# Kernel tuning notes

Measured on AMD Instinct MI355X. Metric: run time of the kernel, lower is better.

Reference implementation:

```python
import jax, jax.numpy as jnp
import numpy as np

N_NODES = 50000
C = 256          # in_channels == hidden_size
E = 800000


def setup_inputs() -> dict:
    key = jax.random.key(0)
    ks = jax.random.split(key, 12)
    x = jax.random.normal(ks[0], (N_NODES, C), dtype=jnp.float32)
    edge_index = jax.random.randint(ks[1], (2, E), 0, N_NODES, dtype=jnp.int64)
    edge_attr = jax.random.uniform(ks[2], (E,), dtype=jnp.float32)
    edge_weights_index = jax.random.randint(ks[3], (2, E), 0, N_NODES, dtype=jnp.int64)
    s = 1.0 / np.sqrt(C)
    # TopKPooling projection vector
    p_pool = jax.random.normal(ks[4], (C,), dtype=jnp.float32) * s
    # GRU (input=C, hidden=C): gates stacked [r, z, n]
    W_ih = jax.random.normal(ks[5], (3 * C, C), dtype=jnp.float32) * s
    W_hh = jax.random.normal(ks[6], (3 * C, C), dtype=jnp.float32) * s
    b_ih = jnp.zeros((3 * C,), dtype=jnp.float32)
    b_hh = jnp.zeros((3 * C,), dtype=jnp.float32)
    # initial evolving GCN weight [C, C]
    W_init = jax.random.normal(ks[7], (C, C), dtype=jnp.float32) * s
    # EdgeDecoder MLP
    lin1_w = jax.random.normal(ks[8], (C, 2 * C), dtype=jnp.float32) / np.sqrt(2 * C)
    lin1_b = jnp.zeros((C,), dtype=jnp.float32)
    lin2_w = jax.random.normal(ks[9], (1, C), dtype=jnp.float32) * s
    lin2_b = jnp.zeros((1,), dtype=jnp.float32)
    return {
        "x": x, "edge_index": edge_index, "edge_attr": edge_attr,
        "edge_weights_index": edge_weights_index,
        "p_pool": p_pool, "W_ih": W_ih, "W_hh": W_hh, "b_ih": b_ih, "b_hh": b_hh,
        "W_init": W_init, "lin1_w": lin1_w, "lin1_b": lin1_b,
        "lin2_w": lin2_w, "lin2_b": lin2_b,
    }


def _forward(x, edge_attr, p_pool, W_ih, W_hh, b_ih, b_hh, W_init,
             lin1_w, lin1_b, lin2_w, lin2_b, edge_index, edge_weights_index):
    n_nodes, c = x.shape
    # --- EvolveGCNH: TopK pooling summary (k = in_channels) ---
    score = x @ p_pool / jnp.linalg.norm(p_pool)          # [N]
    top_score, perm = jax.lax.top_k(score, c)             # [C]
    x_tilde = x[perm] * jnp.tanh(top_score)[:, None]      # [C, C]
    # --- GRU step: input x_tilde (batch=C), hidden = evolving weight W_init ---
    gi = x_tilde @ W_ih.T + b_ih                           # [C, 3C]
    gh = W_init @ W_hh.T + b_hh                            # [C, 3C]
    i_r, i_z, i_n = jnp.split(gi, 3, axis=1)
    h_r, h_z, h_n = jnp.split(gh, 3, axis=1)
    r = jax.nn.sigmoid(i_r + h_r)
    z = jax.nn.sigmoid(i_z + h_z)
    n = jnp.tanh(i_n + r * h_n)
    W = (1.0 - z) * n + z * W_init                         # [C, C] evolved GCN weight
    # --- GCNConv with fixed W, add_self_loops=False ---
    xw = x @ W                                             # [N, C]
    src, dst = edge_index[0], edge_index[1]
    deg = jax.ops.segment_sum(edge_attr, dst, num_segments=n_nodes)
    dinv = jnp.where(deg > 0, jax.lax.rsqrt(jnp.where(deg > 0, deg, 1.0)), 0.0)
    norm = dinv[src] * edge_attr * dinv[dst]               # [E]
    node_emb = jax.ops.segment_sum(xw[src] * norm[:, None], dst,
                                   num_segments=n_nodes)   # [N, C]
    # --- EdgeDecoder: gather src/trg, concat, MLP ---
    s_idx, t_idx = edge_weights_index[0], edge_weights_index[1]
    edge_emb = jnp.concatenate([node_emb[s_idx], node_emb[t_idx]], axis=1)  # [E, 2C]
    h = jax.nn.relu(edge_emb @ lin1_w.T + lin1_b)          # [E, C]
    pred = h @ lin2_w.T + lin2_b                           # [E, 1]
    return pred.reshape(-1)


def reference(x, edge_index, edge_attr, edge_weights_index, p_pool,
              W_ih, W_hh, b_ih, b_hh, W_init, lin1_w, lin1_b, lin2_w, lin2_b):
    # dropout is identity in eval mode
    return _forward(x, edge_attr, p_pool, W_ih, W_hh, b_ih, b_hh, W_init,
                    lin1_w, lin1_b, lin2_w, lin2_b, edge_index, edge_weights_index)
```

## Files before the change

kernel.cpp:

```cpp
#include <hip/hip_runtime.h>
#include <hip/hip_bf16.h>
#include <math.h>


typedef __attribute__((ext_vector_type(8))) short bf16x8;
typedef __attribute__((ext_vector_type(8))) unsigned short u16x8;
typedef __attribute__((ext_vector_type(4))) float f32x4;

#define WSHIFT 9
#define WMASK 511
#define NBUCK 98

__device__ __forceinline__ unsigned f2key(float f) {
  unsigned u = __float_as_uint(f);
  return (u & 0x80000000u) ? ~u : (u | 0x80000000u);
}

__device__ __forceinline__ unsigned short f2bf(float f) {
  unsigned u = __float_as_uint(f);
  unsigned r = u + 0x7fffu + ((u >> 16) & 1u);
  return (unsigned short)(r >> 16);
}
__device__ __forceinline__ float bf2f(unsigned short h) {
  return __uint_as_float((unsigned)h << 16);
}

template <int CTRL>
__device__ __forceinline__ float dpp_add(float s) {
  int t = __builtin_amdgcn_update_dpp(0, __float_as_int(s), CTRL, 0xf, 0xf, false);
  return s + __int_as_float(t);
}

__device__ __forceinline__ void gload16(const void* g, void* l) {
  __builtin_amdgcn_global_load_lds((const __attribute__((address_space(1))) void*)g,
                                   (__attribute__((address_space(3))) void*)l, 16, 0, 0);
}

__global__ __launch_bounds__(256) void init_kernel(const float* __restrict__ lin1,
                                                   unsigned short* __restrict__ WAB,
                                                   int4* __restrict__ zb, int nz4) {
  int b = blockIdx.x, tid = threadIdx.x;
  if (b < 512) {
    int idx = b * 256 + tid;
    int n = idx >> 9, k = idx & 511;
    unsigned short h = f2bf(lin1[idx]);
    if (k < 256)
      WAB[n * 256 + k] = h;
    else
      WAB[(256 + n) * 256 + (k - 256)] = h;
  } else {
    int j = (b - 512) * 256 + tid;
    if (j < nz4) zb[j] = make_int4(0, 0, 0, 0);
  }
}

__global__ __launch_bounds__(256) void fusedA_kernel(const float* __restrict__ x,
                                                     const float* __restrict__ p,
                                                     float* __restrict__ score,
                                                     unsigned short* __restrict__ xh, int N,
                                                     const int* __restrict__ ei,
                                                     const int* __restrict__ ewi,
                                                     int* __restrict__ bcnt1,
                                                     int* __restrict__ bcnt2, int E) {
  int tid = threadIdx.x;
  if (blockIdx.x < 256) {
    __shared__ int c1[128], c2[128];
    if (tid < 128) { c1[tid] = 0; c2[tid] = 0; }
    __syncthreads();
    int idx = blockIdx.x * 256 + tid;
    int stride = 256 * 256;
    for (int e = idx; e < E; e += stride) {
      atomicAdd(&c1[ei[E + e] >> WSHIFT], 1);
      atomicAdd(&c2[ewi[e] >> WSHIFT], 1);
    }
    __syncthreads();
    if (tid < 128) {
      if (c1[tid]) atomicAdd(&bcnt1[tid], c1[tid]);
      if (c2[tid]) atomicAdd(&bcnt2[tid], c2[tid]);
    }
  } else {
    int node = (blockIdx.x - 256) * 4 + (tid >> 6);
    int lane = tid & 63;
    if (node >= N) return;
    float4 xv = ((const float4*)(x + (size_t)node * 256))[lane];
    ushort4 hv;
    hv.x = f2bf(xv.x);
    hv.y = f2bf(xv.y);
    hv.z = f2bf(xv.z);
    hv.w = f2bf(xv.w);
    ((ushort4*)(xh + (size_t)node * 256))[lane] = hv;
    float4 pv = ((const float4*)p)[lane];
    float s = xv.x * pv.x + xv.y * pv.y + xv.z * pv.z + xv.w * pv.w;
    float sp = pv.x * pv.x + pv.y * pv.y + pv.z * pv.z + pv.w * pv.w;
#pragma unroll
    for (int off = 32; off > 0; off >>= 1) {
      s += __shfl_down(s, off, 64);
      sp += __shfl_down(sp, off, 64);
    }
    if (lane == 0) score[node] = s / sqrtf(sp);
  }
}

__global__ __launch_bounds__(256) void fusedB_kernel(const float* __restrict__ score, int n,
                                                     int* __restrict__ gh,
                                                     const int* __restrict__ bcnt1,
                                                     const int* __restrict__ bcnt2,
                                                     int* __restrict__ bbase1,
                                                     int* __restrict__ bbase2,
                                                     int* __restrict__ gcur1,
                                                     int* __restrict__ gcur2,
                                                     int* __restrict__ rowp1,
                                                     int* __restrict__ rowp2, int N, int E) {
  int tid = threadIdx.x;
  if (blockIdx.x < 64) {
    __shared__ int lh[4096];
    for (int i = tid; i < 4096; i += 256) lh[i] = 0;
    __syncthreads();
    int idx = blockIdx.x * 256 + tid;
    int stride = 64 * 256;
    for (int i = idx; i < n; i += stride) {
      unsigned key = f2key(score[i]);
      atomicAdd(&lh[key >> 20], 1);
    }
    __syncthreads();
    for (int i = tid; i < 4096; i += 256) {
      int v = lh[i];
      if (v) atomicAdd(&gh[i], v);
    }
  } else {
    __shared__ int ss[128];
    int v = 0;
    if (tid < 128) { v = (tid < NBUCK) ? bcnt1[tid] : 0; ss[tid] = v; }
    __syncthreads();
    for (int off = 1; off < 128; off <<= 1) {
      int a = 0, b = 0;
      if (tid < 128) { a = ss[tid]; b = (tid >= off) ? ss[tid - off] : 0; }
      __syncthreads();
      if (tid < 128) ss[tid] = a + b;
      __syncthreads();
    }
    if (tid < 128) {
      int excl = ss[tid] - v;
      if (tid < NBUCK) { bbase1[tid] = excl; gcur1[tid] = excl; }
      if (tid == NBUCK - 1) bbase1[NBUCK] = excl + v;
    }
    __syncthreads();
    int v2 = 0;
    if (tid < 128) { v2 = (tid < NBUCK) ? bcnt2[tid] : 0; ss[tid] = v2; }
    __syncthreads();
    for (int off = 1; off < 128; off <<= 1) {
      int a = 0, b = 0;
      if (tid < 128) { a = ss[tid]; b = (tid >= off) ? ss[tid - off] : 0; }
      __syncthreads();
      if (tid < 128) ss[tid] = a + b;
      __syncthreads();
    }
    if (tid < 128) {
      int excl = ss[tid] - v2;
      if (tid < NBUCK) { bbase2[tid] = excl; gcur2[tid] = excl; }
      if (tid == NBUCK - 1) bbase2[NBUCK] = excl + v2;
    }
    if (tid == 0) { rowp1[N] = E; rowp2[N] = E; }
  }
}

__global__ __launch_bounds__(1024) void fusedC_kernel(const int* __restrict__ ei,
                                                      const float* __restrict__ attr,
                                                      int* __restrict__ gcur1,
                                                      int2* __restrict__ stage1,
                                                      const int* __restrict__ ewi,
                                                      int* __restrict__ gcur2,
                                                      int2* __restrict__ stage2,
                                                      int E, int nb,
                                                      const float* __restrict__ score, int n, int k,
                                                      const int* __restrict__ gh,
                                                      int* __restrict__ perm,
                                                      float* __restrict__ tts) {
  int tid = threadIdx.x;
  if ((int)blockIdx.x < 2 * nb) {
    bool conv = (int)blockIdx.x < nb;
    __shared__ int pcnt[128], pcur[128];
    int base = (conv ? blockIdx.x : blockIdx.x - nb) * 8192;
    int* gcur = conv ? gcur1 : gcur2;
    int2* stage = conv ? stage1 : stage2;
    if (tid < 128) pcnt[tid] = 0;
    __syncthreads();
    int bk[8];
    int2 pl[8];
#pragma unroll
    for (int i = 0; i < 8; ++i) {
      int e = base + i * 1024 + tid;
      bk[i] = -1;
      if (e < E) {
        if (conv) {
          int d = ei[E + e];
          int s = ei[e];
          bk[i] = d >> WSHIFT;
          pl[i] = make_int2(s | ((d & WMASK) << 16), __float_as_int(attr[e]));
        } else {
          int s = ewi[e];
          int d = ewi[E + e];
          bk[i] = s >> WSHIFT;
          pl[i] = make_int2(d | ((s & WMASK) << 16), e);
        }
        atomicAdd(&pcnt[bk[i]], 1);
      }
    }
    __syncthreads();
    if (tid < NBUCK) {
      int c = pcnt[tid];
      pcur[tid] = c ? atomicAdd(&gcur[tid], c) : 0;
    }
    __syncthreads();
#pragma unroll
    for (int i = 0; i < 8; ++i) {
      if (bk[i] >= 0) {
        int pos = atomicAdd(&pcur[bk[i]], 1);
        stage[pos] = pl[i];
      }
    }
  } else {
    __shared__ int part[1024];
    __shared__ unsigned sT;
    {
      int b0 = tid * 4;
      int s0 = gh[b0], s1 = gh[b0 + 1], s2 = gh[b0 + 2], s3 = gh[b0 + 3];
      part[tid] = s0 + s1 + s2 + s3;
      __syncthreads();
      for (int off = 1; off < 1024; off <<= 1) {
        int v = part[tid];
        int add = (tid + off < 1024) ? part[tid + off] : 0;
        __syncthreads();
        part[tid] = v + add;
        __syncthreads();
      }
      int sufChunk = part[tid];
      int sufNext = (tid < 1023) ? part[tid + 1] : 0;
      if (sufNext < k && sufChunk >= k) {
        int run = sufNext;
        int b;
        run += s3;
        if (run >= k) b = b0 + 3;
        else {
          run += s2;
          if (run >= k) b = b0 + 2;
          else {
            run += s1;
            b = (run >= k) ? b0 + 1 : b0;
          }
        }
        sT = ((unsigned)b) << 20;
      }
    }
    __syncthreads();
    unsigned T = sT;
    __shared__ unsigned keys[1024];
    __shared__ int idxs[1024];
    __shared__ int cnt;
    if (tid == 0) cnt = 0;
    keys[tid] = 0u;
    idxs[tid] = 0x7fffffff;
    __syncthreads();
    for (int i = tid; i < n; i += 1024) {
      unsigned key = f2key(score[i]);
      if (key >= T) {
        int p = atomicAdd(&cnt, 1);
        if (p < 1024) { keys[p] = key; idxs[p] = i; }
      }
    }
    __syncthreads();
    for (int size = 2; size <= 1024; size <<= 1) {
      for (int stride = size >> 1; stride > 0; stride >>= 1) {
        int j = tid ^ stride;
        if (j > tid) {
          unsigned ka = keys[tid], kb = keys[j];
          int ia = idxs[tid], ib = idxs[j];
          bool aBefore = (ka > kb) || (ka == kb && ia < ib);
          bool up = ((tid & size) == 0);
          if (aBefore != up) {
            keys[tid] = kb; keys[j] = ka;
            idxs[tid] = ib; idxs[j] = ia;
          }
        }
        __syncthreads();
      }
    }
    if (tid < k) {
      int idx = idxs[tid];
      perm[tid] = idx;
      tts[tid] = tanhf(score[idx]);
    }
  }
}

__global__ __launch_bounds__(256) void fusedD_kernel(const float* __restrict__ x,
                                                     const int* __restrict__ perm,
                                                     const float* __restrict__ tts,
                                                     const float* __restrict__ Wi,
                                                     const float* __restrict__ W_ih,
                                                     const float* __restrict__ W_hh,
                                                     const float* __restrict__ b_ih,
                                                     const float* __restrict__ b_hh,
                                                     unsigned short* __restrict__ WevoT,
                                                     const int2* __restrict__ stage1,
                                                     const int* __restrict__ bbase1,
                                                     int2* __restrict__ esv,
                                                     int* __restrict__ rowp1,
                                                     float* __restrict__ dinv,
                                                     const int2* __restrict__ stage2,
                                                     const int* __restrict__ bbase2,
                                                     int2* __restrict__ eto,
                                                     int* __restrict__ rowp2, int N) {
  int tid = threadIdx.x;
  if (blockIdx.x < 256) {
    int i = blockIdx.x, j = tid;
    __shared__ float sx[256], sh[256];
    sx[j] = x[(size_t)perm[i] * 256 + j] * tts[i];
    sh[j] = Wi[i * 256 + j];
    __syncthreads();
    float gi[3], gh[3];
#pragma unroll
    for (int g = 0; g < 3; ++g) {
      int row = g * 256 + j;
      const float4* wi4 = (const float4*)(W_ih + (size_t)row * 256);
      const float4* wh4 = (const float4*)(W_hh + (size_t)row * 256);
      float si = 0.f, s2 = 0.f;
      for (int k4 = 0; k4 < 64; ++k4) {
        float4 wv = wi4[k4];
        float4 hv = wh4[k4];
        int k = k4 * 4;
        si += sx[k] * wv.x + sx[k + 1] * wv.y + sx[k + 2] * wv.z + sx[k + 3] * wv.w;
        s2 += sh[k] * hv.x + sh[k + 1] * hv.y + sh[k + 2] * hv.z + sh[k + 3] * hv.w;
      }
      gi[g] = si + b_ih[row];
      gh[g] = s2 + b_hh[row];
    }
    float r = 1.f / (1.f + expf(-(gi[0] + gh[0])));
    float z = 1.f / (1.f + expf(-(gi[1] + gh[1])));
    float nn = tanhf(gi[2] + r * gh[2]);
    float w = (1.f - z) * nn + z * sh[j];
    WevoT[(size_t)j * 256 + i] = f2bf(w);
  } else {
    __shared__ int cnt[512];
    __shared__ float degs[512];
    __shared__ int pref[512];
    __shared__ int ss[256];
    int bb2 = blockIdx.x - 256;
    bool isConv = bb2 < NBUCK;
    int b = isConv ? bb2 : bb2 - NBUCK;
    const int2* stage = isConv ? stage1 : stage2;
    const int* bbase = isConv ? bbase1 : bbase2;
    int beg = bbase[b], end = bbase[b + 1];
    int node0 = b << WSHIFT;
    cnt[tid] = 0; cnt[tid + 256] = 0;
    degs[tid] = 0.f; degs[tid + 256] = 0.f;
    __syncthreads();
    for (int j = beg + tid; j < end; j += 256) {
      int2 p = stage[j];
      int loc = p.x >> 16;
      atomicAdd(&cnt[loc], 1);
      if (isConv) atomicAdd(&degs[loc], __int_as_float(p.y));
    }
    __syncthreads();
    int c0 = cnt[2 * tid], c1 = cnt[2 * tid + 1];
    ss[tid] = c0 + c1;
    __syncthreads();
    for (int off = 1; off < 256; off <<= 1) {
      int a = ss[tid];
      int bsum = (tid >= off) ? ss[tid - off] : 0;
      __syncthreads();
      ss[tid] = a + bsum;
      __syncthreads();
    }
    int excl = (tid ? ss[tid - 1] : 0);
    pref[2 * tid] = excl;
    pref[2 * tid + 1] = excl + c0;
    __syncthreads();
#pragma unroll
    for (int h = 0; h < 2; ++h) {
      int i = tid + h * 256;
      int node = node0 + i;
      if (node < N) {
        if (isConv) {
          rowp1[node] = beg + pref[i];
          float d = degs[i];
          dinv[node] = d > 0.f ? 1.f / sqrtf(d) : 0.f;
        } else {
          rowp2[node] = beg + pref[i];
        }
      }
    }
    __syncthreads();
    int2* outb = isConv ? esv : eto;
    for (int j = beg + tid; j < end; j += 256) {
      int2 p = stage[j];
      int loc = p.x >> 16;
      int pos = beg + atomicAdd(&pref[loc], 1);
      outb[pos] = make_int2(p.x & 0xFFFF, p.y);
    }
  }
}

__global__ __launch_bounds__(512) void mfma_gemm128(const unsigned short* __restrict__ A,
                                                    const unsigned short* __restrict__ BT,
                                                    unsigned short* __restrict__ C1,
                                                    unsigned short* __restrict__ C2,
                                                    int M) {
  __shared__ unsigned short sA[128 * 32];
  __shared__ unsigned short sB[256 * 32];
  int tid = threadIdx.x;
  int wave = tid >> 6, lane = tid & 63;
  int quad = lane >> 4, r16 = lane & 15;
  int wm = wave >> 2, wn = wave & 3;
  int mbase = blockIdx.x * 128;
  const unsigned short* Bt = BT + ((size_t)blockIdx.y << 16);
  unsigned short* Cout = blockIdx.y ? C2 : C1;

  int srow = tid >> 2, scolq = tid & 3;
  const unsigned short* gA = A + (size_t)(mbase + srow) * 256 + scolq * 8;
  const unsigned short* gB0 = Bt + (size_t)srow * 256 + scolq * 8;
  const unsigned short* gB1 = Bt + (size_t)(128 + srow) * 256 + scolq * 8;
  unsigned short* lA = sA + wave * 512;
  unsigned short* lB0 = sB + wave * 512;
  unsigned short* lB1 = sB + 4096 + wave * 512;

  f32x4 acc[4][4];
#pragma unroll
  for (int i = 0; i < 4; ++i)
#pragma unroll
    for (int j = 0; j < 4; ++j) acc[i][j] = (f32x4){0.f, 0.f, 0.f, 0.f};

  const unsigned short* pA = sA + (wm * 64 + r16) * 32 + quad * 8;
  const unsigned short* pB = sB + (wn * 64 + r16) * 32 + quad * 8;

  for (int k0 = 0; k0 < 256; k0 += 32) {
    if (k0) __syncthreads();
    gload16(gA + k0, lA);
    gload16(gB0 + k0, lB0);
    gload16(gB1 + k0, lB1);
    __syncthreads();
    bf16x8 af[4], bfr[4];
#pragma unroll
    for (int mt = 0; mt < 4; ++mt) af[mt] = *(const bf16x8*)(pA + mt * 512);
#pragma unroll
    for (int nt = 0; nt < 4; ++nt) bfr[nt] = *(const bf16x8*)(pB + nt * 512);
#pragma unroll
    for (int mt = 0; mt < 4; ++mt)
#pragma unroll
      for (int nt = 0; nt < 4; ++nt)
        acc[mt][nt] = __builtin_amdgcn_mfma_f32_16x16x32_bf16(af[mt], bfr[nt], acc[mt][nt], 0, 0, 0);
  }
#pragma unroll
  for (int mt = 0; mt < 4; ++mt) {
#pragma unroll
    for (int rr = 0; rr < 4; ++rr) {
      int grow = mbase + wm * 64 + mt * 16 + quad * 4 + rr;
      if (grow < M) {
#pragma unroll
        for (int nt = 0; nt < 4; ++nt)
          Cout[(size_t)grow * 256 + wn * 64 + nt * 16 + r16] = f2bf(acc[mt][nt][rr]);
      }
    }
  }
}

__global__ __launch_bounds__(256) void gcn_gather(const unsigned short* __restrict__ xw,
                                                  const int* __restrict__ row_ptr,
                                                  const int2* __restrict__ esv,
                                                  const float* __restrict__ dinv,
                                                  unsigned short* __restrict__ ne, int N) {
  int node = blockIdx.x * 4 + (threadIdx.x >> 6);
  int lane = threadIdx.x & 63;
  int g = lane & 15, q = lane >> 4;
  if (node >= N) return;
  int beg = row_ptr[node], end = row_ptr[node + 1];
  float acc[16];
#pragma unroll
  for (int c = 0; c < 16; ++c) acc[c] = 0.f;
  const unsigned short* xb = xw + g * 16;

  for (int cb = beg; cb < end; cb += 64) {
    int cend = cb + 64 < end ? cb + 64 : end;
    int me = cb + lane;
    int2 mm = (me < cend) ? esv[me] : make_int2(0, 0);
    int mx = mm.x;
    float mv = __int_as_float(mm.y) * dinv[mx];

    float vA = 0.f, vB = 0.f, vC = 0.f;
    u16x8 rAa, rAb, rBa, rBb, rCa, rCb;
    {
      int e = cb + q;
      int sx = __shfl(mx, q, 64);
      float tv = __shfl(mv, q, 64);
      vA = (e < cend) ? tv : 0.f;
      rAa = *(const u16x8*)(xb + (size_t)sx * 256);
      rAb = *(const u16x8*)(xb + (size_t)sx * 256 + 8);
    }
    if (cb + 4 < cend) {
      int e = cb + 4 + q;
      int sx = __shfl(mx, 4 + q, 64);
      float tv = __shfl(mv, 4 + q, 64);
      vB = (e < cend) ? tv : 0.f;
      rBa = *(const u16x8*)(xb + (size_t)sx * 256);
      rBb = *(const u16x8*)(xb + (size_t)sx * 256 + 8);
    } else { rBa = rAa; rBb = rAb; }
    if (cb + 8 < cend) {
      int e = cb + 8 + q;
      int sx = __shfl(mx, 8 + q, 64);
      float tv = __shfl(mv, 8 + q, 64);
      vC = (e < cend) ? tv : 0.f;
      rCa = *(const u16x8*)(xb + (size_t)sx * 256);
      rCb = *(const u16x8*)(xb + (size_t)sx * 256 + 8);
    } else { rCa = rAa; rCb = rAb; }

    for (int jb = cb; jb < cend; jb += 12) {
#pragma unroll
      for (int c = 0; c < 8; ++c) acc[c] += bf2f(rAa[c]) * vA;
#pragma unroll
      for (int c = 0; c < 8; ++c) acc[8 + c] += bf2f(rAb[c]) * vA;
      vA = 0.f;
      if (jb + 12 < cend) {
        int e = jb + 12 + q;
        int idx = (e - cb) & 63;
        int sx = __shfl(mx, idx, 64);
        float tv = __shfl(mv, idx, 64);
        vA = (e < cend) ? tv : 0.f;
        rAa = *(const u16x8*)(xb + (size_t)sx * 256);
        rAb = *(const u16x8*)(xb + (size_t)sx * 256 + 8);
      }
#pragma unroll
      for (int c = 0; c < 8; ++c) acc[c] += bf2f(rBa[c]) * vB;
#pragma unroll
      for (int c = 0; c < 8; ++c) acc[8 + c] += bf2f(rBb[c]) * vB;
      vB = 0.f;
      if (jb + 16 < cend) {
        int e = jb + 16 + q;
        int idx = (e - cb) & 63;
        int sx = __shfl(mx, idx, 64);
        float tv = __shfl(mv, idx, 64);
        vB = (e < cend) ? tv : 0.f;
        rBa = *(const u16x8*)(xb + (size_t)sx * 256);
        rBb = *(const u16x8*)(xb + (size_t)sx * 256 + 8);
      }
#pragma unroll
      for (int c = 0; c < 8; ++c) acc[c] += bf2f(rCa[c]) * vC;
#pragma unroll
      for (int c = 0; c < 8; ++c) acc[8 + c] += bf2f(rCb[c]) * vC;
      vC = 0.f;
      if (jb + 20 < cend) {
        int e = jb + 20 + q;
        int idx = (e - cb) & 63;
        int sx = __shfl(mx, idx, 64);
        float tv = __shfl(mv, idx, 64);
        vC = (e < cend) ? tv : 0.f;
        rCa = *(const u16x8*)(xb + (size_t)sx * 256);
        rCb = *(const u16x8*)(xb + (size_t)sx * 256 + 8);
      }
    }
  }
#pragma unroll
  for (int c = 0; c < 16; ++c) {
    acc[c] += __shfl_xor(acc[c], 16, 64);
    acc[c] += __shfl_xor(acc[c], 32, 64);
  }
  if (q == 0) {
    float dd = dinv[node];
    u16x8 o0, o1;
#pragma unroll
    for (int c = 0; c < 8; ++c) {
      o0[c] = f2bf(acc[c] * dd);
      o1[c] = f2bf(acc[8 + c] * dd);
    }
    *(u16x8*)(ne + (size_t)node * 256 + g * 16) = o0;
    *(u16x8*)(ne + (size_t)node * 256 + g * 16 + 8) = o1;
  }
}

__global__ __launch_bounds__(256) void edge_decode_csr(const unsigned short* __restrict__ A,
                                                       const unsigned short* __restrict__ Bm,
                                                       const int* __restrict__ row_ptr,
                                                       const int2* __restrict__ eto,
                                                       const float* __restrict__ b1,
                                                       const float* __restrict__ w2,
                                                       const float* __restrict__ b2,
                                                       float* __restrict__ out, int N) {
  int node = blockIdx.x * 4 + (threadIdx.x >> 6);
  int lane = threadIdx.x & 63;
  int g = lane & 15, q = lane >> 4;
  if (node >= N) return;
  int beg = row_ptr[node], end = row_ptr[node + 1];
  if (beg >= end) return;
  float a[16], w[16];
  {
    u16x8 a0 = *(const u16x8*)(A + (size_t)node * 256 + g * 16);
    u16x8 a1 = *(const u16x8*)(A + (size_t)node * 256 + g * 16 + 8);
    const float4* bp = (const float4*)(b1 + g * 16);
    const float4* wp = (const float4*)(w2 + g * 16);
#pragma unroll
    for (int i = 0; i < 4; ++i) {
      float4 bv = bp[i];
      float4 wv = wp[i];
      a[i * 4 + 0] = (i < 2 ? bf2f(a0[i * 4 + 0]) : bf2f(a1[i * 4 - 8])) + bv.x;
      a[i * 4 + 1] = (i < 2 ? bf2f(a0[i * 4 + 1]) : bf2f(a1[i * 4 - 7])) + bv.y;
      a[i * 4 + 2] = (i < 2 ? bf2f(a0[i * 4 + 2]) : bf2f(a1[i * 4 - 6])) + bv.z;
      a[i * 4 + 3] = (i < 2 ? bf2f(a0[i * 4 + 3]) : bf2f(a1[i * 4 - 5])) + bv.w;
      w[i * 4 + 0] = wv.x;
      w[i * 4 + 1] = wv.y;
      w[i * 4 + 2] = wv.z;
      w[i * 4 + 3] = wv.w;
    }
  }
  float base = b2[0];
  const unsigned short* Bb = Bm + g * 16;

  for (int cb = beg; cb < end; cb += 64) {
    int cend = cb + 64 < end ? cb + 64 : end;
    int me = cb + lane;
    int2 mm = (me < cend) ? eto[me] : make_int2(0, 0);
    int mx = mm.x, my = mm.y;

    bool okA = false, okB = false, okC = false;
    int oA = 0, oB = 0, oC = 0;
    u16x8 rAa, rAb, rBa, rBb, rCa, rCb;
    {
      int e = cb + q;
      int sx = __shfl(mx, q, 64);
      oA = __shfl(my, q, 64);
      okA = e < cend;
      rAa = *(const u16x8*)(Bb + (size_t)sx * 256);
      rAb = *(const u16x8*)(Bb + (size_t)sx * 256 + 8);
    }
    if (cb + 4 < cend) {
      int e = cb + 4 + q;
      int sx = __shfl(mx, 4 + q, 64);
      oB = __shfl(my, 4 + q, 64);
      okB = e < cend;
      rBa = *(const u16x8*)(Bb + (size_t)sx * 256);
      rBb = *(const u16x8*)(Bb + (size_t)sx * 256 + 8);
    } else { rBa = rAa; rBb = rAb; }
    if (cb + 8 < cend) {
      int e = cb + 8 + q;
      int sx = __shfl(mx, 8 + q, 64);
      oC = __shfl(my, 8 + q, 64);
      okC = e < cend;
      rCa = *(const u16x8*)(Bb + (size_t)sx * 256);
      rCb = *(const u16x8*)(Bb + (size_t)sx * 256 + 8);
    } else { rCa = rAa; rCb = rAb; }

    for (int jb = cb; jb < cend; jb += 12) {
      {
        float s0 = 0.f, s1 = 0.f;
#pragma unroll
        for (int c = 0; c < 8; ++c) s0 += fmaxf(a[c] + bf2f(rAa[c]), 0.f) * w[c];
#pragma unroll
        for (int c = 0; c < 8; ++c) s1 += fmaxf(a[8 + c] + bf2f(rAb[c]), 0.f) * w[8 + c];
        float s = s0 + s1;
        s = dpp_add<0x128>(s);
        s = dpp_add<0x124>(s);
        s = dpp_add<0x122>(s);
        s = dpp_add<0x121>(s);
        if (g == 0 && okA) out[oA] = s + base;
      }
      okA = false;
      if (jb + 12 < cend) {
        int e = jb + 12 + q;
        int idx = (e - cb) & 63;
        int sx = __shfl(mx, idx, 64);
        oA = __shfl(my, idx, 64);
        okA = e < cend;
        rAa = *(const u16x8*)(Bb + (size_t)sx * 256);
        rAb = *(const u16x8*)(Bb + (size_t)sx * 256 + 8);
      }
      {
        float s0 = 0.f, s1 = 0.f;
#pragma unroll
        for (int c = 0; c < 8; ++c) s0 += fmaxf(a[c] + bf2f(rBa[c]), 0.f) * w[c];
#pragma unroll
        for (int c = 0; c < 8; ++c) s1 += fmaxf(a[8 + c] + bf2f(rBb[c]), 0.f) * w[8 + c];
        float s = s0 + s1;
        s = dpp_add<0x128>(s);
        s = dpp_add<0x124>(s);
        s = dpp_add<0x122>(s);
        s = dpp_add<0x121>(s);
        if (g == 0 && okB) out[oB] = s + base;
      }
      okB = false;
      if (jb + 16 < cend) {
        int e = jb + 16 + q;
        int idx = (e - cb) & 63;
        int sx = __shfl(mx, idx, 64);
        oB = __shfl(my, idx, 64);
        okB = e < cend;
        rBa = *(const u16x8*)(Bb + (size_t)sx * 256);
        rBb = *(const u16x8*)(Bb + (size_t)sx * 256 + 8);
      }
      {
        float s0 = 0.f, s1 = 0.f;
#pragma unroll
        for (int c = 0; c < 8; ++c) s0 += fmaxf(a[c] + bf2f(rCa[c]), 0.f) * w[c];
#pragma unroll
        for (int c = 0; c < 8; ++c) s1 += fmaxf(a[8 + c] + bf2f(rCb[c]), 0.f) * w[8 + c];
        float s = s0 + s1;
        s = dpp_add<0x128>(s);
        s = dpp_add<0x124>(s);
        s = dpp_add<0x122>(s);
        s = dpp_add<0x121>(s);
        if (g == 0 && okC) out[oC] = s + base;
      }
      okC = false;
      if (jb + 20 < cend) {
        int e = jb + 20 + q;
        int idx = (e - cb) & 63;
        int sx = __shfl(mx, idx, 64);
        oC = __shfl(my, idx, 64);
        okC = e < cend;
        rCa = *(const u16x8*)(Bb + (size_t)sx * 256);
        rCb = *(const u16x8*)(Bb + (size_t)sx * 256 + 8);
      }
    }
  }
}

extern "C" void kernel_launch(void* const* d_in, const int* in_sizes, int n_in,
                              void* d_out, int out_size, void* d_ws, size_t ws_size,
                              hipStream_t stream) {
  const float* x      = (const float*)d_in[0];
  const int*   ei     = (const int*)d_in[1];
  const float* attr   = (const float*)d_in[2];
  const int*   ewi    = (const int*)d_in[3];
  const float* p_pool = (const float*)d_in[4];
  const float* W_ih   = (const float*)d_in[5];
  const float* W_hh   = (const float*)d_in[6];
  const float* b_ih   = (const float*)d_in[7];
  const float* b_hh   = (const float*)d_in[8];
  const float* W_init = (const float*)d_in[9];
  const float* lin1_w = (const float*)d_in[10];
  const float* lin1_b = (const float*)d_in[11];
  const float* lin2_w = (const float*)d_in[12];
  const float* lin2_b = (const float*)d_in[13];
  float* out = (float*)d_out;

  const int C = 256;
  const int N = in_sizes[0] / C;
  const int E = in_sizes[2];

  char* ws = (char*)d_ws;
  size_t off = 0;
  auto alloc = [&](size_t bytes) {
    size_t o = off;
    off = (off + bytes + 255) & ~(size_t)255;
    return o;
  };
  float*          score  = (float*)(ws + alloc((size_t)N * 4));
  int*            perm   = (int*)(ws + alloc(C * 4));
  float*          tts    = (float*)(ws + alloc(C * 4));
  unsigned short* WevoT  = (unsigned short*)(ws + alloc((size_t)C * C * 2));
  unsigned short* WAB    = (unsigned short*)(ws + alloc((size_t)2 * C * C * 2));
  int   zeroInts = 4096 + 128 + 128;
  char* zbase    = ws + alloc((size_t)zeroInts * 4);
  int* ghist = (int*)zbase;
  int* bcnt1 = (int*)(zbase + 4096 * 4);
  int* bcnt2 = (int*)(zbase + 4096 * 4 + 128 * 4);
  int*            bbase1 = (int*)(ws + alloc((NBUCK + 1) * 4));
  int*            bbase2 = (int*)(ws + alloc((NBUCK + 1) * 4));
  int*            gcur1  = (int*)(ws + alloc(128 * 4));
  int*            gcur2  = (int*)(ws + alloc(128 * 4));
  float*          dinv   = (float*)(ws + alloc((size_t)N * 4));
  int*            rowp1  = (int*)(ws + alloc((size_t)(N + 1) * 4));
  int*            rowp2  = (int*)(ws + alloc((size_t)(N + 1) * 4));
  int2*           stage1 = (int2*)(ws + alloc((size_t)E * 8));
  int2*           stage2 = (int2*)(ws + alloc((size_t)E * 8));
  int2*           esv    = (int2*)(ws + alloc((size_t)E * 8));
  int2*           eto    = (int2*)(ws + alloc((size_t)E * 8));
  unsigned short* xh     = (unsigned short*)(ws + alloc((size_t)N * C * 2));
  unsigned short* xwh    = (unsigned short*)(ws + alloc((size_t)N * C * 2));
  unsigned short* Bbf    = (unsigned short*)(ws + alloc((size_t)N * C * 2));
  unsigned short* ne  = xh;
  unsigned short* Abf = xwh;

  int nz4 = (zeroInts + 3) / 4;
  int nbP1 = (E + 8191) / 8192;

  init_kernel<<<512 + (nz4 + 255) / 256, 256, 0, stream>>>(lin1_w, WAB, (int4*)zbase, nz4);

  fusedA_kernel<<<256 + (N + 3) / 4, 256, 0, stream>>>(x, p_pool, score, xh, N,
                                                       ei, ewi, bcnt1, bcnt2, E);

  fusedB_kernel<<<65, 256, 0, stream>>>(score, N, ghist, bcnt1, bcnt2,
                                        bbase1, bbase2, gcur1, gcur2,
                                        rowp1, rowp2, N, E);

  fusedC_kernel<<<2 * nbP1 + 1, 1024, 0, stream>>>(ei, attr, gcur1, stage1,
                                                   ewi, gcur2, stage2, E, nbP1,
                                                   score, N, C, ghist, perm, tts);

  fusedD_kernel<<<256 + 2 * NBUCK, 256, 0, stream>>>(x, perm, tts, W_init,
                                                     W_ih, W_hh, b_ih, b_hh, WevoT,
                                                     stage1, bbase1, esv, rowp1, dinv,
                                                     stage2, bbase2, eto, rowp2, N);

  mfma_gemm128<<<dim3((N + 127) / 128, 1), 512, 0, stream>>>(xh, WevoT, xwh, xwh, N);

  gcn_gather<<<(N + 3) / 4, 256, 0, stream>>>(xwh, rowp1, esv, dinv, ne, N);

  mfma_gemm128<<<dim3((N + 127) / 128, 2), 512, 0, stream>>>(ne, WAB, Abf, Bbf, N);

  edge_decode_csr<<<(N + 3) / 4, 256, 0, stream>>>(Abf, Bbf, rowp2, eto,
                                                   lin1_b, lin2_w, lin2_b, out, N);
}
```

Measured before the change: 405.6 us.

## Reassociate GCN and decoder GEMMs, fold evolved weight into lin1, drop atomics

The GCN aggregation now runs on raw bf16 x instead of x@W, and the evolved weight W is folded into the decoder's lin1 halves via a small 256x256 product (PAB = lin1_half·W). This removes one full N×C GEMM pass and its intermediate buffer. The init kernel is merged into fusedA, and the global atomic histograms are replaced by per-block partial histograms that are summed later. This removes the zeroing step and the atomic contention, at the cost of extra reads in fusedB and fusedC and different bf16 rounding order.

Measured after the change: 447.8 us. 1.1x slower.

```diff
diff --git a/kernel.cpp b/kernel.cpp
--- a/kernel.cpp
+++ b/kernel.cpp
@@ -36,50 +36,20 @@
                                    (__attribute__((address_space(3))) void*)l, 16, 0, 0);
 }
 
-__global__ __launch_bounds__(256) void init_kernel(const float* __restrict__ lin1,
-                                                   unsigned short* __restrict__ WAB,
-                                                   int4* __restrict__ zb, int nz4) {
-  int b = blockIdx.x, tid = threadIdx.x;
-  if (b < 512) {
-    int idx = b * 256 + tid;
-    int n = idx >> 9, k = idx & 511;
-    unsigned short h = f2bf(lin1[idx]);
-    if (k < 256)
-      WAB[n * 256 + k] = h;
-    else
-      WAB[(256 + n) * 256 + (k - 256)] = h;
-  } else {
-    int j = (b - 512) * 256 + tid;
-    if (j < nz4) zb[j] = make_int4(0, 0, 0, 0);
-  }
-}
-
 __global__ __launch_bounds__(256) void fusedA_kernel(const float* __restrict__ x,
                                                      const float* __restrict__ p,
                                                      float* __restrict__ score,
-                                                     unsigned short* __restrict__ xh, int N,
+                                                     unsigned short* __restrict__ xh, int N, int NS,
                                                      const int* __restrict__ ei,
                                                      const int* __restrict__ ewi,
-                                                     int* __restrict__ bcnt1,
-                                                     int* __restrict__ bcnt2, int E) {
+                                                     int* __restrict__ bh1p,
+                                                     int* __restrict__ bh2p, int E,
+                                                     const float* __restrict__ lin1,
+                                                     unsigned short* __restrict__ WAB) {
   int tid = threadIdx.x;
-  if (blockIdx.x < 256) {
-    __shared__ int c1[128], c2[128];
-    if (tid < 128) { c1[tid] = 0; c2[tid] = 0; }
-    __syncthreads();
-    int idx = blockIdx.x * 256 + tid;
-    int stride = 256 * 256;
-    for (int e = idx; e < E; e += stride) {
-      atomicAdd(&c1[ei[E + e] >> WSHIFT], 1);
-      atomicAdd(&c2[ewi[e] >> WSHIFT], 1);
-    }
-    __syncthreads();
-    if (tid < 128) {
-      if (c1[tid]) atomicAdd(&bcnt1[tid], c1[tid]);
-      if (c2[tid]) atomicAdd(&bcnt2[tid], c2[tid]);
-    }
-  } else {
-    int node = (blockIdx.x - 256) * 4 + (tid >> 6);
+  int b = blockIdx.x;
+  if (b < NS) {
+    int node = b * 4 + (tid >> 6);
     int lane = tid & 63;
     if (node >= N) return;
     float4 xv = ((const float4*)(x + (size_t)node * 256))[lane];
@@ -98,13 +68,37 @@
       sp += __shfl_down(sp, off, 64);
     }
     if (lane == 0) score[node] = s / sqrtf(sp);
+  } else if (b < NS + 256) {
+    __shared__ int c1[128], c2[128];
+    int bb = b - NS;
+    if (tid < 128) { c1[tid] = 0; c2[tid] = 0; }
+    __syncthreads();
+    int idx = bb * 256 + tid;
+    int stride = 256 * 256;
+    for (int e = idx; e < E; e += stride) {
+      atomicAdd(&c1[ei[E + e] >> WSHIFT], 1);
+      atomicAdd(&c2[ewi[e] >> WSHIFT], 1);
+    }
+    __syncthreads();
+    if (tid < 128) {
+      bh1p[bb * 128 + tid] = c1[tid];
+      bh2p[bb * 128 + tid] = c2[tid];
+    }
+  } else {
+    int idx = (b - NS - 256) * 256 + tid;
+    int n = idx >> 9, k = idx & 511;
+    unsigned short h = f2bf(lin1[idx]);
+    if (k < 256)
+      WAB[n * 256 + k] = h;
+    else
+      WAB[(256 + n) * 256 + (k - 256)] = h;
   }
 }
 
 __global__ __launch_bounds__(256) void fusedB_kernel(const float* __restrict__ score, int n,
-                                                     int* __restrict__ gh,
-                                                     const int* __restrict__ bcnt1,
-                                                     const int* __restrict__ bcnt2,
+                                                     int* __restrict__ ghp,
+                                                     const int* __restrict__ bh1p,
+                                                     const int* __restrict__ bh2p,
                                                      int* __restrict__ bbase1,
                                                      int* __restrict__ bbase2,
                                                      int* __restrict__ gcur1,
@@ -123,20 +117,22 @@
       atomicAdd(&lh[key >> 20], 1);
     }
     __syncthreads();
-    for (int i = tid; i < 4096; i += 256) {
-      int v = lh[i];
-      if (v) atomicAdd(&gh[i], v);
-    }
+    int* row = ghp + blockIdx.x * 4096;
+    for (int i = tid; i < 4096; i += 256) row[i] = lh[i];
   } else {
     __shared__ int ss[128];
     int v = 0;
-    if (tid < 128) { v = (tid < NBUCK) ? bcnt1[tid] : 0; ss[tid] = v; }
+    if (tid < 128) {
+      if (tid < NBUCK)
+        for (int r = 0; r < 256; ++r) v += bh1p[r * 128 + tid];
+      ss[tid] = v;
+    }
     __syncthreads();
     for (int off = 1; off < 128; off <<= 1) {
-      int a = 0, b = 0;
-      if (tid < 128) { a = ss[tid]; b = (tid >= off) ? ss[tid - off] : 0; }
+      int a = 0, bsum = 0;
+      if (tid < 128) { a = ss[tid]; bsum = (tid >= off) ? ss[tid - off] : 0; }
       __syncthreads();
-      if (tid < 128) ss[tid] = a + b;
+      if (tid < 128) ss[tid] = a + bsum;
       __syncthreads();
     }
     if (tid < 128) {
@@ -146,13 +142,17 @@
     }
     __syncthreads();
     int v2 = 0;
-    if (tid < 128) { v2 = (tid < NBUCK) ? bcnt2[tid] : 0; ss[tid] = v2; }
+    if (tid < 128) {
+      if (tid < NBUCK)
+        for (int r = 0; r < 256; ++r) v2 += bh2p[r * 128 + tid];
+      ss[tid] = v2;
+    }
     __syncthreads();
     for (int off = 1; off < 128; off <<= 1) {
-      int a = 0, b = 0;
-      if (tid < 128) { a = ss[tid]; b = (tid >= off) ? ss[tid - off] : 0; }
+      int a = 0, bsum = 0;
+      if (tid < 128) { a = ss[tid]; bsum = (tid >= off) ? ss[tid - off] : 0; }
       __syncthreads();
-      if (tid < 128) ss[tid] = a + b;
+      if (tid < 128) ss[tid] = a + bsum;
       __syncthreads();
     }
     if (tid < 128) {
@@ -173,7 +173,7 @@
                                                       int2* __restrict__ stage2,
                                                       int E, int nb,
                                                       const float* __restrict__ score, int n, int k,
-                                                      const int* __restrict__ gh,
+                                                      const int* __restrict__ ghp,
                                                       int* __restrict__ perm,
                                                       float* __restrict__ tts) {
   int tid = threadIdx.x;
@@ -222,9 +222,14 @@
   } else {
     __shared__ int part[1024];
     __shared__ unsigned sT;
+    int s0, s1, s2, s3;
     {
       int b0 = tid * 4;
-      int s0 = gh[b0], s1 = gh[b0 + 1], s2 = gh[b0 + 2], s3 = gh[b0 + 3];
+      s0 = 0; s1 = 0; s2 = 0; s3 = 0;
+      for (int r = 0; r < 64; ++r) {
+        int4 v4 = *(const int4*)(ghp + r * 4096 + b0);
+        s0 += v4.x; s1 += v4.y; s2 += v4.z; s3 += v4.w;
+      }
       part[tid] = s0 + s1 + s2 + s3;
       __syncthreads();
       for (int off = 1; off < 1024; off <<= 1) {
@@ -240,13 +245,13 @@
         int run = sufNext;
         int b;
         run += s3;
-        if (run >= k) b = b0 + 3;
+        if (run >= k) b = tid * 4 + 3;
         else {
           run += s2;
-          if (run >= k) b = b0 + 2;
+          if (run >= k) b = tid * 4 + 2;
           else {
             run += s1;
-            b = (run >= k) ? b0 + 1 : b0;
+            b = (run >= k) ? tid * 4 + 1 : tid * 4;
           }
         }
         sT = ((unsigned)b) << 20;
@@ -301,7 +306,7 @@
                                                      const float* __restrict__ W_hh,
                                                      const float* __restrict__ b_ih,
                                                      const float* __restrict__ b_hh,
-                                                     unsigned short* __restrict__ WevoT,
+                                                     unsigned short* __restrict__ Wr,
                                                      const int2* __restrict__ stage1,
                                                      const int* __restrict__ bbase1,
                                                      int2* __restrict__ esv,
@@ -339,7 +344,7 @@
     float z = 1.f / (1.f + expf(-(gi[1] + gh[1])));
     float nn = tanhf(gi[2] + r * gh[2]);
     float w = (1.f - z) * nn + z * sh[j];
-    WevoT[(size_t)j * 256 + i] = f2bf(w);
+    Wr[(size_t)i * 256 + j] = f2bf(w);
   } else {
     __shared__ int cnt[512];
     __shared__ float degs[512];
@@ -401,83 +406,63 @@
   }
 }
 
-__global__ __launch_bounds__(512) void mfma_gemm128(const unsigned short* __restrict__ A,
-                                                    const unsigned short* __restrict__ BT,
-                                                    unsigned short* __restrict__ C1,
-                                                    unsigned short* __restrict__ C2,
-                                                    int M) {
-  __shared__ unsigned short sA[128 * 32];
-  __shared__ unsigned short sB[256 * 32];
+__global__ __launch_bounds__(256) void fusedE_kernel(const unsigned short* __restrict__ xh,
+                                                     const int* __restrict__ row_ptr,
+                                                     const int2* __restrict__ esv,
+                                                     const float* __restrict__ dinv,
+                                                     unsigned short* __restrict__ agg, int N, int NSB,
+                                                     const unsigned short* __restrict__ WAB,
+                                                     const unsigned short* __restrict__ Wr,
+                                                     unsigned short* __restrict__ PAB) {
   int tid = threadIdx.x;
-  int wave = tid >> 6, lane = tid & 63;
-  int quad = lane >> 4, r16 = lane & 15;
-  int wm = wave >> 2, wn = wave & 3;
-  int mbase = blockIdx.x * 128;
-  const unsigned short* Bt = BT + ((size_t)blockIdx.y << 16);
-  unsigned short* Cout = blockIdx.y ? C2 : C1;
-
-  int srow = tid >> 2, scolq = tid & 3;
-  const unsigned short* gA = A + (size_t)(mbase + srow) * 256 + scolq * 8;
-  const unsigned short* gB0 = Bt + (size_t)srow * 256 + scolq * 8;
-  const unsigned short* gB1 = Bt + (size_t)(128 + srow) * 256 + scolq * 8;
-  unsigned short* lA = sA + wave * 512;
-  unsigned short* lB0 = sB + wave * 512;
-  unsigned short* lB1 = sB + 4096 + wave * 512;
-
-  f32x4 acc[4][4];
-#pragma unroll
-  for (int i = 0; i < 4; ++i)
-#pragma unroll
-    for (int j = 0; j < 4; ++j) acc[i][j] = (f32x4){0.f, 0.f, 0.f, 0.f};
-
-  const unsigned short* pA = sA + (wm * 64 + r16) * 32 + quad * 8;
-  const unsigned short* pB = sB + (wn * 64 + r16) * 32 + quad * 8;
-
-  for (int k0 = 0; k0 < 256; k0 += 32) {
-    if (k0) __syncthreads();
-    gload16(gA + k0, lA);
-    gload16(gB0 + k0, lB0);
-    gload16(gB1 + k0, lB1);
-    __syncthreads();
-    bf16x8 af[4], bfr[4];
-#pragma unroll
-    for (int mt = 0; mt < 4; ++mt) af[mt] = *(const bf16x8*)(pA + mt * 512);
-#pragma unroll
-    for (int nt = 0; nt < 4; ++nt) bfr[nt] = *(const bf16x8*)(pB + nt * 512);
+  int lane = tid & 63;
+  if ((int)blockIdx.x >= NSB) {
+    int cb = blockIdx.x - NSB;
+    int by = cb >> 2, mb = cb & 3;
+    int wave = tid >> 6;
+    int quad = lane >> 4, r16 = lane & 15;
+    int n0 = wave * 64;
+    int mbase = mb * 64;
+    const unsigned short* A = WAB + ((size_t)by << 16);
+    f32x4 acc[4][4];
+#pragma unroll
+    for (int i = 0; i < 4; ++i)
+#pragma unroll
+      for (int j = 0; j < 4; ++j) acc[i][j] = (f32x4){0.f, 0.f, 0.f, 0.f};
+    for (int k0 = 0; k0 < 256; k0 += 32) {
+      int koff = k0 + quad * 8;
+      bf16x8 af[4], bfr[4];
+#pragma unroll
+      for (int mt = 0; mt < 4; ++mt)
+        af[mt] = *(const bf16x8*)(A + (size_t)(mbase + mt * 16 + r16) * 256 + koff);
+#pragma unroll
+      for (int nt = 0; nt < 4; ++nt)
+        bfr[nt] = *(const bf16x8*)(Wr + (size_t)(n0 + nt * 16 + r16) * 256 + koff);
+#pragma unroll
+      for (int mt = 0; mt < 4; ++mt)
+#pragma unroll
+        for (int nt = 0; nt < 4; ++nt)
+          acc[mt][nt] = __builtin_amdgcn_mfma_f32_16x16x32_bf16(af[mt], bfr[nt], acc[mt][nt], 0, 0, 0);
+    }
 #pragma unroll
     for (int mt = 0; mt < 4; ++mt)
 #pragma unroll
-      for (int nt = 0; nt < 4; ++nt)
-        acc[mt][nt] = __builtin_amdgcn_mfma_f32_16x16x32_bf16(af[mt], bfr[nt], acc[mt][nt], 0, 0, 0);
-  }
-#pragma unroll
-  for (int mt = 0; mt < 4; ++mt) {
-#pragma unroll
-    for (int rr = 0; rr < 4; ++rr) {
-      int grow = mbase + wm * 64 + mt * 16 + quad * 4 + rr;
-      if (grow < M) {
+      for (int rr = 0; rr < 4; ++rr) {
+        int grow = mbase + mt * 16 + (lane >> 4) * 4 + rr;
 #pragma unroll
         for (int nt = 0; nt < 4; ++nt)
-          Cout[(size_t)grow * 256 + wn * 64 + nt * 16 + r16] = f2bf(acc[mt][nt][rr]);
-      }
-    }
-  }
-}
-
-__global__ __launch_bounds__(256) void gcn_gather(const unsigned short* __restrict__ xw,
-                                                  const int* __restrict__ row_ptr,
-                                                  const int2* __restrict__ esv,
-                                                  const float* __restrict__ dinv,
-                                                  unsigned short* __restrict__ ne, int N) {
-  int node = blockIdx.x * 4 + (threadIdx.x >> 6);
-  int lane = threadIdx.x & 63;
+          PAB[(size_t)(by * 256 + grow) * 256 + n0 + nt * 16 + r16] = f2bf(acc[mt][nt][rr]);
+      }
+    return;
+  }
+  int node = blockIdx.x * 4 + (tid >> 6);
   int g = lane & 15, q = lane >> 4;
   if (node >= N) return;
   int beg = row_ptr[node], end = row_ptr[node + 1];
   float acc[16];
 #pragma unroll
   for (int c = 0; c < 16; ++c) acc[c] = 0.f;
-  const unsigned short* xb = xw + g * 16;
+  const unsigned short* xb = xh + g * 16;
 
   for (int cb = beg; cb < end; cb += 64) {
     int cend = cb + 64 < end ? cb + 64 : end;
@@ -571,8 +556,71 @@
       o0[c] = f2bf(acc[c] * dd);
       o1[c] = f2bf(acc[8 + c] * dd);
     }
-    *(u16x8*)(ne + (size_t)node * 256 + g * 16) = o0;
-    *(u16x8*)(ne + (size_t)node * 256 + g * 16 + 8) = o1;
+    *(u16x8*)(agg + (size_t)node * 256 + g * 16) = o0;
+    *(u16x8*)(agg + (size_t)node * 256 + g * 16 + 8) = o1;
+  }
+}
+
+__global__ __launch_bounds__(512) void mfma_gemm128(const unsigned short* __restrict__ A,
+                                                    const unsigned short* __restrict__ BT,
+                                                    unsigned short* __restrict__ C1,
+                                                    unsigned short* __restrict__ C2,
+                                                    int M) {
+  __shared__ unsigned short sA[128 * 32];
+  __shared__ unsigned short sB[256 * 32];
+  int tid = threadIdx.x;
+  int wave = tid >> 6, lane = tid & 63;
+  int quad = lane >> 4, r16 = lane & 15;
+  int wm = wave >> 2, wn = wave & 3;
+  int mbase = blockIdx.x * 128;
+  const unsigned short* Bt = BT + ((size_t)blockIdx.y << 16);
+  unsigned short* Cout = blockIdx.y ? C2 : C1;
+
+  int srow = tid >> 2, scolq = tid & 3;
+  const unsigned short* gA = A + (size_t)(mbase + srow) * 256 + scolq * 8;
+  const unsigned short* gB0 = Bt + (size_t)srow * 256 + scolq * 8;
+  const unsigned short* gB1 = Bt + (size_t)(128 + srow) * 256 + scolq * 8;
+  unsigned short* lA = sA + wave * 512;
+  unsigned short* lB0 = sB + wave * 512;
+  unsigned short* lB1 = sB + 4096 + wave * 512;
+
+  f32x4 acc[4][4];
+#pragma unroll
+  for (int i = 0; i < 4; ++i)
+#pragma unroll
+    for (int j = 0; j < 4; ++j) acc[i][j] = (f32x4){0.f, 0.f, 0.f, 0.f};
+
+  const unsigned short* pA = sA + (wm * 64 + r16) * 32 + quad * 8;
+  const unsigned short* pB = sB + (wn * 64 + r16) * 32 + quad * 8;
+
+  for (int k0 = 0; k0 < 256; k0 += 32) {
+    if (k0) __syncthreads();
+    gload16(gA + k0, lA);
+    gload16(gB0 + k0, lB0);
+    gload16(gB1 + k0, lB1);
+    __syncthreads();
+    bf16x8 af[4], bfr[4];
+#pragma unroll
+    for (int mt = 0; mt < 4; ++mt) af[mt] = *(const bf16x8*)(pA + mt * 512);
+#pragma unroll
+    for (int nt = 0; nt < 4; ++nt) bfr[nt] = *(const bf16x8*)(pB + nt * 512);
+#pragma unroll
+    for (int mt = 0; mt < 4; ++mt)
+#pragma unroll
+      for (int nt = 0; nt < 4; ++nt)
+        acc[mt][nt] = __builtin_amdgcn_mfma_f32_16x16x32_bf16(af[mt], bfr[nt], acc[mt][nt], 0, 0, 0);
+  }
+#pragma unroll
+  for (int mt = 0; mt < 4; ++mt) {
+#pragma unroll
+    for (int rr = 0; rr < 4; ++rr) {
+      int grow = mbase + wm * 64 + mt * 16 + quad * 4 + rr;
+      if (grow < M) {
+#pragma unroll
+        for (int nt = 0; nt < 4; ++nt)
+          Cout[(size_t)grow * 256 + wn * 64 + nt * 16 + r16] = f2bf(acc[mt][nt][rr]);
+      }
+    }
   }
 }
 
@@ -754,13 +802,12 @@
   float*          score  = (float*)(ws + alloc((size_t)N * 4));
   int*            perm   = (int*)(ws + alloc(C * 4));
   float*          tts    = (float*)(ws + alloc(C * 4));
-  unsigned short* WevoT  = (unsigned short*)(ws + alloc((size_t)C * C * 2));
+  unsigned short* Wr     = (unsigned short*)(ws + alloc((size_t)C * C * 2));
   unsigned short* WAB    = (unsigned short*)(ws + alloc((size_t)2 * C * C * 2));
-  int   zeroInts = 4096 + 128 + 128;
-  char* zbase    = ws + alloc((size_t)zeroInts * 4);
-  int* ghist = (int*)zbase;
-  int* bcnt1 = (int*)(zbase + 4096 * 4);
-  int* bcnt2 = (int*)(zbase + 4096 * 4 + 128 * 4);
+  unsigned short* PAB    = (unsigned short*)(ws + alloc((size_t)2 * C * C * 2));
+  int*            bh1p   = (int*)(ws + alloc((size_t)256 * 128 * 4));
+  int*            bh2p   = (int*)(ws + alloc((size_t)256 * 128 * 4));
+  int*            ghp    = (int*)(ws + alloc((size_t)64 * 4096 * 4));
   int*            bbase1 = (int*)(ws + alloc((NBUCK + 1) * 4));
   int*            bbase2 = (int*)(ws + alloc((NBUCK + 1) * 4));
   int*            gcur1  = (int*)(ws + alloc(128 * 4));
@@ -773,38 +820,35 @@
   int2*           esv    = (int2*)(ws + alloc((size_t)E * 8));
   int2*           eto    = (int2*)(ws + alloc((size_t)E * 8));
   unsigned short* xh     = (unsigned short*)(ws + alloc((size_t)N * C * 2));
-  unsigned short* xwh    = (unsigned short*)(ws + alloc((size_t)N * C * 2));
+  unsigned short* agg    = (unsigned short*)(ws + alloc((size_t)N * C * 2));
   unsigned short* Bbf    = (unsigned short*)(ws + alloc((size_t)N * C * 2));
-  unsigned short* ne  = xh;
-  unsigned short* Abf = xwh;
-
-  int nz4 = (zeroInts + 3) / 4;
+  unsigned short* Abf = xh;
+
+  int NS = (N + 3) / 4;
   int nbP1 = (E + 8191) / 8192;
 
-  init_kernel<<<512 + (nz4 + 255) / 256, 256, 0, stream>>>(lin1_w, WAB, (int4*)zbase, nz4);
-
-  fusedA_kernel<<<256 + (N + 3) / 4, 256, 0, stream>>>(x, p_pool, score, xh, N,
-                                                       ei, ewi, bcnt1, bcnt2, E);
-
-  fusedB_kernel<<<65, 256, 0, stream>>>(score, N, ghist, bcnt1, bcnt2,
+  fusedA_kernel<<<NS + 256 + 512, 256, 0, stream>>>(x, p_pool, score, xh, N, NS,
+                                                    ei, ewi, bh1p, bh2p, E,
+                                                    lin1_w, WAB);
+
+  fusedB_kernel<<<65, 256, 0, stream>>>(score, N, ghp, bh1p, bh2p,
                                         bbase1, bbase2, gcur1, gcur2,
                                         rowp1, rowp2, N, E);
 
   fusedC_kernel<<<2 * nbP1 + 1, 1024, 0, stream>>>(ei, attr, gcur1, stage1,
                                                    ewi, gcur2, stage2, E, nbP1,
-                                                   score, N, C, ghist, perm, tts);
+                                                   score, N, C, ghp, perm, tts);
 
   fusedD_kernel<<<256 + 2 * NBUCK, 256, 0, stream>>>(x, perm, tts, W_init,
-                                                     W_ih, W_hh, b_ih, b_hh, WevoT,
+                                                     W_ih, W_hh, b_ih, b_hh, Wr,
                                                      stage1, bbase1, esv, rowp1, dinv,
                                                      stage2, bbase2, eto, rowp2, N);
 
-  mfma_gemm128<<<dim3((N + 127) / 128, 1), 512, 0, stream>>>(xh, WevoT, xwh, xwh, N);
-
-  gcn_gather<<<(N + 3) / 4, 256, 0, stream>>>(xwh, rowp1, esv, dinv, ne, N);
-
-  mfma_gemm128<<<dim3((N + 127) / 128, 2), 512, 0, stream>>>(ne, WAB, Abf, Bbf, N);
-
-  edge_decode_csr<<<(N + 3) / 4, 256, 0, stream>>>(Abf, Bbf, rowp2, eto,
-                                                   lin1_b, lin2_w, lin2_b, out, N);
-}
+  fusedE_kernel<<<NS + 8, 256, 0, stream>>>(xh, rowp1, esv, dinv, agg, N, NS,
+                                            WAB, Wr, PAB);
+
+  mfma_gemm128<<<dim3((N + 127) / 128, 2), 512, 0, stream>>>(agg, PAB, Abf, Bbf, N);
+
+  edge_decode_csr<<<NS, 256, 0, stream>>>(Abf, Bbf, rowp2, eto,
+                                          lin1_b, lin2_w, lin2_b, out, N);
+}
```
